# Kernel optimization log

Measured on AMD Instinct MI355X. Metric: run time of the kernel, lower is better.

## Reference

```python
import jax, jax.numpy as jnp
import numpy as np

# Module constants (match init_kwargs)
IMG_W = 384
IMG_H = 384
DECAY = 0.97
VEH_W = 2.1
VEH_L = 4.9
PPM = 5
LIGHT_OFF_X = 12.0
LIGHT_OFF_Y = 3.25
ALPHA = 1.1


def create_coordinate_mask(nx, ny, ppm):
    # Metric coordinates of every BEV pixel, ego frame origin at image center.
    xs = (jnp.arange(nx, dtype=jnp.float32) - nx / 2.0) / ppm
    ys = (jnp.arange(ny, dtype=jnp.float32) - ny / 2.0) / ppm
    X, Y = jnp.meshgrid(xs, ys)  # (ny, nx)
    return jnp.stack([X, Y], axis=-1)  # (H, W, 2)


def rotate_batched(location, yaw):
    # Express future poses (t=1..T-1) in the frame of the pose at t=0.
    loc0 = location[:, :1]              # (B,1,2)
    yaw0 = yaw[:, :1]                   # (B,1,1)
    rel = location[:, 1:] - loc0        # (B,T-1,2)
    c, s = jnp.cos(yaw0), jnp.sin(yaw0)
    x = c * rel[..., 0:1] + s * rel[..., 1:2]    # (B,T-1,1)
    y = -s * rel[..., 0:1] + c * rel[..., 1:2]   # (B,T-1,1)
    return x, y, yaw[:, 1:] - yaw0


def align_with_ego(x, y, yaw, cm):
    # Translate grid to ego position then rotate into ego heading frame.
    # x,y,yaw: (B,T-1,1); cm: (H,W,2). Returns two (B,T-1,H,W) coord fields.
    relx = cm[..., 0][None, None] - x[..., None]   # (B,T-1,H,W)
    rely = cm[..., 1][None, None] - y[..., None]
    c = jnp.cos(yaw)[..., None]
    s = jnp.sin(yaw)[..., None]
    ax = c * relx + s * rely
    ay = -s * relx + c * rely
    return ax, ay


def calculate_mask(ax, ay, dx, dy, vw, vl, alpha):
    dtype = ax.dtype
    # Speed-dependent corridor ahead of the vehicle.
    mask_car = ((jnp.abs(ax) <= dx) & (ay >= 0.0) & (ay <= dy)).astype(dtype)
    # Inflated vehicle footprint (for lane / offroad costs).
    mask_side = ((jnp.abs(ax) <= alpha * vw / 2.0)
                 & (jnp.abs(ay) <= alpha * vl / 2.0)).astype(dtype)
    return mask_car, mask_side


def setup_inputs() -> dict:
    key = jax.random.key(0)
    k1, k2, k3, k4 = jax.random.split(key, 4)
    B, T = 8, 11
    location = jax.random.normal(k1, (B, T, 2), dtype=jnp.float32) * 5.0
    yaw = jax.random.normal(k2, (B, T, 1), dtype=jnp.float32) * 0.3
    speed = jax.random.uniform(k3, (B, T, 1), dtype=jnp.float32) * 15.0
    bev = jax.random.uniform(k4, (B, T, 8, IMG_H, IMG_W), dtype=jnp.float32)
    return {"location": location, "yaw": yaw, "speed": speed, "bev": bev}


def reference(location, yaw, speed, bev):
    cm = create_coordinate_mask(IMG_W, IMG_H, PPM)   # (H,W,2)
    x, y, yaw_ = rotate_batched(location, yaw)        # (B,T-1,1) each
    speed_ = speed[:, 1:, 0:1]                        # (B,T-1,1)

    ax, ay = align_with_ego(x, y, yaw_, cm)
    axl, ayl = align_with_ego(x + LIGHT_OFF_X, y + LIGHT_OFF_Y, yaw_, cm)

    dx = VEH_W / 2.0 + 4.0
    dx_light = VEH_W + 1.0
    dy = (1.5 * (jnp.maximum(10.0, speed_) + VEH_L) + 1.0)[..., None]  # (B,T-1,1,1)
    dy_light = (speed_ * 0.5 + VEH_L * 3.0)[..., None]                  # (B,T-1,1,1)

    mask_car, mask_side = calculate_mask(ax, ay, dx, dy, VEH_W, VEH_L, ALPHA)
    mask_light, _ = calculate_mask(axl, ayl, dx_light, dy_light, VEH_W, VEH_L, ALPHA)

    # Binarize BEV at 0.5 (matches the in-place > / <= thresholding).
    bev_b = (bev[:, 1:] > 0.5).astype(bev.dtype)  # (B,T-1,8,H,W)

    Tm1 = bev_b.shape[1]
    decay = jnp.power(jnp.float32(DECAY),
                      jnp.arange(Tm1, dtype=jnp.float32)).reshape(1, Tm1, 1, 1)

    def cost(chan, mask):
        return jnp.sum(bev_b[:, :, chan] * mask * decay)

    lane_cost = cost(1, mask_side)
    vehicle_cost = cost(2, mask_car)
    green_light_cost = cost(3, mask_light)
    yellow_light_cost = cost(4, mask_light)
    red_light_cost = cost(5, mask_light)
    pedestrian_cost = cost(6, mask_car)
    offroad_cost = cost(7, mask_side)

    return (lane_cost, vehicle_cost, green_light_cost, yellow_light_cost,
            red_light_cost, pedestrian_cost, offroad_cost,
            mask_car, mask_side, mask_light)
```

## Files before the change

kernel.cpp:

```cpp
#include <hip/hip_runtime.h>
#include <math.h>

constexpr int IMG     = 384;
constexpr int NPIX    = IMG * IMG;
constexpr int TM1     = 10;
constexpr int NIMG    = 80;
constexpr int THREADS = 256;
constexpr int GPT     = 4;
constexpr int GPB     = THREADS * GPT;
constexpr int NGRP    = NPIX / 4;
constexpr int NBX     = NGRP / GPB;
constexpr int NSUM    = 12;
constexpr long long NMASK = (long long)NIMG * NPIX;

typedef float v4f __attribute__((ext_vector_type(4)));


__global__ __launch_bounds__(THREADS) void cost_main(
    const float* __restrict__ loc,
    const float* __restrict__ yaw,
    const float* __restrict__ speed,
    const float* __restrict__ bev,
    float* __restrict__ out)
{
    const int img = blockIdx.y;
    const int b   = img / TM1;
    const int t   = img - b * TM1;
    const int tid = threadIdx.x;

    const float yaw0 = yaw[b * 11];
    const float c0 = cosf(yaw0), s0 = sinf(yaw0);
    const float rx = loc[(b * 11 + t + 1) * 2 + 0] - loc[b * 22 + 0];
    const float ry = loc[(b * 11 + t + 1) * 2 + 1] - loc[b * 22 + 1];
    const float x0 =  c0 * rx + s0 * ry;
    const float y0 = -s0 * rx + c0 * ry;
    const float yw = yaw[b * 11 + t + 1] - yaw0;
    const float c = cosf(yw), s = sinf(yw);
    const float sp  = speed[b * 11 + t + 1];
    const float dy  = 1.5f * (fmaxf(10.0f, sp) + 4.9f) + 1.0f;
    const float dyl = sp * 0.5f + 14.7f;
    const float ox  = 12.0f * c + 3.25f * s;
    const float oy  = 12.0f * s - 3.25f * c;

    if (blockIdx.x < NBX) {
        float* ocar   = out + 7 + (size_t)img * NPIX;
        float* oside  = ocar + NMASK;
        float* olight = ocar + 2 * NMASK;

        const int g0 = blockIdx.x * GPB + tid;
        #pragma unroll
        for (int it = 0; it < GPT; ++it) {
            const int g = g0 + it * THREADS;
            if (g != NGRP - 1) {
                const int pb = 4 * g + 1;
                float mc[4], ms[4], ml[4];
                #pragma unroll
                for (int k = 0; k < 4; ++k) {
                    const int p = pb + k;
                    const int i = p / IMG;
                    const int j = p - i * IMG;
                    const float X = (float)j * 0.2f - 38.4f;
                    const float Y = (float)i * 0.2f - 38.4f;
                    const float relx = X - x0, rely = Y - y0;
                    const float ax = c * relx + s * rely;
                    const float ay = c * rely - s * relx;
                    const float axl = ax - ox, ayl = ay + oy;
                    mc[k] = (fabsf(ax)  <= 5.05f  && ay >= 0.f && ay <= dy)   ? 1.f : 0.f;
                    ms[k] = (fabsf(ax)  <= 1.155f && fabsf(ay) <= 2.695f)     ? 1.f : 0.f;
                    ml[k] = (fabsf(axl) <= 3.1f   && ayl >= 0.f && ayl <= dyl)? 1.f : 0.f;
                }
                v4f vc = {mc[0], mc[1], mc[2], mc[3]};
                v4f vs = {ms[0], ms[1], ms[2], ms[3]};
                v4f vl = {ml[0], ml[1], ml[2], ml[3]};
                *(v4f*)(ocar + pb)   = vc;
                *(v4f*)(oside + pb)  = vs;
                *(v4f*)(olight + pb) = vl;
            } else {
                const int pp[4] = {0, NPIX - 3, NPIX - 2, NPIX - 1};
                for (int k = 0; k < 4; ++k) {
                    const int p = pp[k];
                    const int i = p / IMG;
                    const int j = p - i * IMG;
                    const float X = (float)j * 0.2f - 38.4f;
                    const float Y = (float)i * 0.2f - 38.4f;
                    const float relx = X - x0, rely = Y - y0;
                    const float ax = c * relx + s * rely;
                    const float ay = c * rely - s * relx;
                    const float axl = ax - ox, ayl = ay + oy;
                    ocar[p]   = (fabsf(ax)  <= 5.05f  && ay >= 0.f && ay <= dy)    ? 1.f : 0.f;
                    oside[p]  = (fabsf(ax)  <= 1.155f && fabsf(ay) <= 2.695f)      ? 1.f : 0.f;
                    olight[p] = (fabsf(axl) <= 3.1f   && ayl >= 0.f && ayl <= dyl) ? 1.f : 0.f;
                }
            }
        }
        return;
    }

    const int q   = blockIdx.x - NBX;
    const int reg = q >> 2;
    const int z   = q & 3;

    const float* bp = bev + (size_t)((b * 11 + t + 1) * 8) * NPIX;

    float u0, u1, v0, v1;
    if (reg == 0)      { u0 = -5.05f;      u1 = 5.05f;      v0 = 0.f;      v1 = dy; }
    else if (reg == 1) { u0 = -1.155f;     u1 = 1.155f;     v0 = -2.695f;  v1 = 2.695f; }
    else               { u0 = ox - 3.1f;   u1 = ox + 3.1f;  v0 = -oy;      v1 = dyl - oy; }

    float Xmn = 1e30f, Xmx = -1e30f, Ymn = 1e30f, Ymx = -1e30f;
    #pragma unroll
    for (int cu = 0; cu < 2; ++cu)
        #pragma unroll
        for (int cv = 0; cv < 2; ++cv) {
            const float u = cu ? u1 : u0, v = cv ? v1 : v0;
            const float X = x0 + c * u - s * v;
            const float Y = y0 + s * u + c * v;
            Xmn = fminf(Xmn, X); Xmx = fmaxf(Xmx, X);
            Ymn = fminf(Ymn, Y); Ymx = fmaxf(Ymx, Y);
        }
    const int j0 = max(0, (int)floorf((Xmn + 38.4f) * 5.f) - 1);
    const int j1 = min(IMG - 1, (int)ceilf((Xmx + 38.4f) * 5.f) + 1);
    const int i0 = max(0, (int)floorf((Ymn + 38.4f) * 5.f) - 1);
    const int i1 = min(IMG - 1, (int)ceilf((Ymx + 38.4f) * 5.f) + 1);

    float a0 = 0.f, a1 = 0.f, a2 = 0.f;

    if (j1 >= j0 && i1 >= i0) {
        const int w = j1 - j0 + 1;
        const int n = w * (i1 - i0 + 1);
        for (int idx = tid + z * THREADS; idx < n; idx += 4 * THREADS) {
            const int ii = idx / w;
            const int jj = j0 + (idx - ii * w);
            const int i  = i0 + ii;
            const float X = (float)jj * 0.2f - 38.4f;
            const float Y = (float)i  * 0.2f - 38.4f;
            const float relx = X - x0, rely = Y - y0;
            const float ax = c * relx + s * rely;
            const float ay = c * rely - s * relx;
            const int p = i * IMG + jj;
            if (reg == 0) {
                if (fabsf(ax) <= 5.05f && ay >= 0.f && ay <= dy) {
                    a0 += (bp[2 * NPIX + p] > 0.5f) ? 1.f : 0.f;
                    a1 += (bp[6 * NPIX + p] > 0.5f) ? 1.f : 0.f;
                }
            } else if (reg == 1) {
                if (fabsf(ax) <= 1.155f && fabsf(ay) <= 2.695f) {
                    a0 += (bp[1 * NPIX + p] > 0.5f) ? 1.f : 0.f;
                    a1 += (bp[7 * NPIX + p] > 0.5f) ? 1.f : 0.f;
                }
            } else {
                const float axl = ax - ox, ayl = ay + oy;
                if (fabsf(axl) <= 3.1f && ayl >= 0.f && ayl <= dyl) {
                    a0 += (bp[3 * NPIX + p] > 0.5f) ? 1.f : 0.f;
                    a1 += (bp[4 * NPIX + p] > 0.5f) ? 1.f : 0.f;
                    a2 += (bp[5 * NPIX + p] > 0.5f) ? 1.f : 0.f;
                }
            }
        }
    }

    float acc[3] = {a0, a1, a2};
    #pragma unroll
    for (int k = 0; k < 3; ++k) {
        #pragma unroll
        for (int off = 32; off > 0; off >>= 1)
            acc[k] += __shfl_down(acc[k], off, 64);
    }
    __shared__ float red[4][3];
    const int wid = tid >> 6, lane = tid & 63;
    if (lane == 0) {
        #pragma unroll
        for (int k = 0; k < 3; ++k) red[wid][k] = acc[k];
    }
    __syncthreads();
    if (tid < 3) {
        const float v = red[0][tid] + red[1][tid] + red[2][tid] + red[3][tid];
        if (v != 0.0f) {
            float decay = 1.0f;
            for (int qd = 0; qd < t; ++qd) decay *= 0.97f;
            int slot;
            if (reg == 0)      slot = (tid == 0) ? 1 : 5;
            else if (reg == 1) slot = (tid == 0) ? 0 : 6;
            else               slot = 2 + tid;
            if (reg == 2 || tid < 2)
                atomicAdd(&out[slot], v * decay);
        }
    }
}

extern "C" void kernel_launch(void* const* d_in, const int* in_sizes, int n_in,
                              void* d_out, int out_size, void* d_ws, size_t ws_size,
                              hipStream_t stream) {
    const float* loc   = (const float*)d_in[0];
    const float* yaw   = (const float*)d_in[1];
    const float* speed = (const float*)d_in[2];
    const float* bev   = (const float*)d_in[3];
    float* out = (float*)d_out;

    (void)hipMemsetAsync(d_out, 0, 7 * sizeof(float), stream);

    dim3 grid(NBX + NSUM, NIMG);
    cost_main<<<grid, THREADS, 0, stream>>>(loc, yaw, speed, bev, out);
}
```

Measured before the change: 38.33 us.

## Replace dense mask writes with memset plus sparse writes inside bounding boxes

Drops the dense pass that evaluated and wrote every pixel of the three mask outputs. Instead the whole output buffer is zeroed with hipMemsetAsync, and the region-sum blocks write 1.0 only for the pixels inside each mask while they accumulate costs. The grid becomes images x regions x 4 slices. Mask writes are now scattered, uncoalesced stores, and the memset still has to write the full ~35 MB output, so the write bandwidth cost remains, just moved to the memset path.

```diff
diff --git a/kernel.cpp b/kernel.cpp
--- a/kernel.cpp
+++ b/kernel.cpp
@@ -6,24 +6,19 @@
 constexpr int TM1     = 10;
 constexpr int NIMG    = 80;
 constexpr int THREADS = 256;
-constexpr int GPT     = 4;
-constexpr int GPB     = THREADS * GPT;
-constexpr int NGRP    = NPIX / 4;
-constexpr int NBX     = NGRP / GPB;
-constexpr int NSUM    = 12;
 constexpr long long NMASK = (long long)NIMG * NPIX;
 
-typedef float v4f __attribute__((ext_vector_type(4)));
 
-
-__global__ __launch_bounds__(THREADS) void cost_main(
+__global__ __launch_bounds__(THREADS) void cost_regions(
     const float* __restrict__ loc,
     const float* __restrict__ yaw,
     const float* __restrict__ speed,
     const float* __restrict__ bev,
     float* __restrict__ out)
 {
-    const int img = blockIdx.y;
+    const int img = blockIdx.x;
+    const int reg = blockIdx.y;
+    const int z   = blockIdx.z;
     const int b   = img / TM1;
     const int t   = img - b * TM1;
     const int tid = threadIdx.x;
@@ -42,65 +37,8 @@
     const float ox  = 12.0f * c + 3.25f * s;
     const float oy  = 12.0f * s - 3.25f * c;
 
-    if (blockIdx.x < NBX) {
-        float* ocar   = out + 7 + (size_t)img * NPIX;
-        float* oside  = ocar + NMASK;
-        float* olight = ocar + 2 * NMASK;
-
-        const int g0 = blockIdx.x * GPB + tid;
-        #pragma unroll
-        for (int it = 0; it < GPT; ++it) {
-            const int g = g0 + it * THREADS;
-            if (g != NGRP - 1) {
-                const int pb = 4 * g + 1;
-                float mc[4], ms[4], ml[4];
-                #pragma unroll
-                for (int k = 0; k < 4; ++k) {
-                    const int p = pb + k;
-                    const int i = p / IMG;
-                    const int j = p - i * IMG;
-                    const float X = (float)j * 0.2f - 38.4f;
-                    const float Y = (float)i * 0.2f - 38.4f;
-                    const float relx = X - x0, rely = Y - y0;
-                    const float ax = c * relx + s * rely;
-                    const float ay = c * rely - s * relx;
-                    const float axl = ax - ox, ayl = ay + oy;
-                    mc[k] = (fabsf(ax)  <= 5.05f  && ay >= 0.f && ay <= dy)   ? 1.f : 0.f;
-                    ms[k] = (fabsf(ax)  <= 1.155f && fabsf(ay) <= 2.695f)     ? 1.f : 0.f;
-                    ml[k] = (fabsf(axl) <= 3.1f   && ayl >= 0.f && ayl <= dyl)? 1.f : 0.f;
-                }
-                v4f vc = {mc[0], mc[1], mc[2], mc[3]};
-                v4f vs = {ms[0], ms[1], ms[2], ms[3]};
-                v4f vl = {ml[0], ml[1], ml[2], ml[3]};
-                *(v4f*)(ocar + pb)   = vc;
-                *(v4f*)(oside + pb)  = vs;
-                *(v4f*)(olight + pb) = vl;
-            } else {
-                const int pp[4] = {0, NPIX - 3, NPIX - 2, NPIX - 1};
-                for (int k = 0; k < 4; ++k) {
-                    const int p = pp[k];
-                    const int i = p / IMG;
-                    const int j = p - i * IMG;
-                    const float X = (float)j * 0.2f - 38.4f;
-                    const float Y = (float)i * 0.2f - 38.4f;
-                    const float relx = X - x0, rely = Y - y0;
-                    const float ax = c * relx + s * rely;
-                    const float ay = c * rely - s * relx;
-                    const float axl = ax - ox, ayl = ay + oy;
-                    ocar[p]   = (fabsf(ax)  <= 5.05f  && ay >= 0.f && ay <= dy)    ? 1.f : 0.f;
-                    oside[p]  = (fabsf(ax)  <= 1.155f && fabsf(ay) <= 2.695f)      ? 1.f : 0.f;
-                    olight[p] = (fabsf(axl) <= 3.1f   && ayl >= 0.f && ayl <= dyl) ? 1.f : 0.f;
-                }
-            }
-        }
-        return;
-    }
-
-    const int q   = blockIdx.x - NBX;
-    const int reg = q >> 2;
-    const int z   = q & 3;
-
     const float* bp = bev + (size_t)((b * 11 + t + 1) * 8) * NPIX;
+    float* op = out + 7 + (size_t)img * NPIX + (size_t)reg * NMASK;
 
     float u0, u1, v0, v1;
     if (reg == 0)      { u0 = -5.05f;      u1 = 5.05f;      v0 = 0.f;      v1 = dy; }
@@ -140,17 +78,20 @@
             const int p = i * IMG + jj;
             if (reg == 0) {
                 if (fabsf(ax) <= 5.05f && ay >= 0.f && ay <= dy) {
+                    op[p] = 1.0f;
                     a0 += (bp[2 * NPIX + p] > 0.5f) ? 1.f : 0.f;
                     a1 += (bp[6 * NPIX + p] > 0.5f) ? 1.f : 0.f;
                 }
             } else if (reg == 1) {
                 if (fabsf(ax) <= 1.155f && fabsf(ay) <= 2.695f) {
+                    op[p] = 1.0f;
                     a0 += (bp[1 * NPIX + p] > 0.5f) ? 1.f : 0.f;
                     a1 += (bp[7 * NPIX + p] > 0.5f) ? 1.f : 0.f;
                 }
             } else {
                 const float axl = ax - ox, ayl = ay + oy;
                 if (fabsf(axl) <= 3.1f && ayl >= 0.f && ayl <= dyl) {
+                    op[p] = 1.0f;
                     a0 += (bp[3 * NPIX + p] > 0.5f) ? 1.f : 0.f;
                     a1 += (bp[4 * NPIX + p] > 0.5f) ? 1.f : 0.f;
                     a2 += (bp[5 * NPIX + p] > 0.5f) ? 1.f : 0.f;
@@ -197,8 +138,8 @@
     const float* bev   = (const float*)d_in[3];
     float* out = (float*)d_out;
 
-    (void)hipMemsetAsync(d_out, 0, 7 * sizeof(float), stream);
+    (void)hipMemsetAsync(d_out, 0, (size_t)out_size * sizeof(float), stream);
 
-    dim3 grid(NBX + NSUM, NIMG);
-    cost_main<<<grid, THREADS, 0, stream>>>(loc, yaw, speed, bev, out);
+    dim3 grid(NIMG, 3, 4);
+    cost_regions<<<grid, THREADS, 0, stream>>>(loc, yaw, speed, bev, out);
 }
```

Measured after the change: 42.77 us. 11.6% more time.

## Flatten grid, schedule reduction blocks first and coarsen mask-writer blocks

Applied to the files above, without the earlier changes.

Replaces the 2D grid with a 1D grid in which all 960 bbox-reduction blocks come first and are dispatched early, followed by mask-writing blocks that each process four chunks instead of one. Putting the latency-bound gather/reduction blocks at the front lets them overlap with the bandwidth-bound mask stores instead of trailing behind them. Coarsening cuts the mask block count by four, at the cost of recomputing the per-image pose parameters (including sin/cos) in every unit and leaving fewer blocks to hide latency.

```diff
diff --git a/kernel.cpp b/kernel.cpp
--- a/kernel.cpp
+++ b/kernel.cpp
@@ -9,8 +9,11 @@
 constexpr int GPT     = 4;
 constexpr int GPB     = THREADS * GPT;
 constexpr int NGRP    = NPIX / 4;
-constexpr int NBX     = NGRP / GPB;
-constexpr int NSUM    = 12;
+constexpr int CHUNKS  = NGRP / GPB;
+constexpr int NUNITS  = NIMG * CHUNKS;
+constexpr int UPB     = 4;
+constexpr int NSTRB   = NUNITS / UPB;
+constexpr int NSUMB   = NIMG * 12;
 constexpr long long NMASK = (long long)NIMG * NPIX;
 
 typedef float v4f __attribute__((ext_vector_type(4)));
@@ -23,31 +26,147 @@
     const float* __restrict__ bev,
     float* __restrict__ out)
 {
-    const int img = blockIdx.y;
-    const int b   = img / TM1;
-    const int t   = img - b * TM1;
     const int tid = threadIdx.x;
 
-    const float yaw0 = yaw[b * 11];
-    const float c0 = cosf(yaw0), s0 = sinf(yaw0);
-    const float rx = loc[(b * 11 + t + 1) * 2 + 0] - loc[b * 22 + 0];
-    const float ry = loc[(b * 11 + t + 1) * 2 + 1] - loc[b * 22 + 1];
-    const float x0 =  c0 * rx + s0 * ry;
-    const float y0 = -s0 * rx + c0 * ry;
-    const float yw = yaw[b * 11 + t + 1] - yaw0;
-    const float c = cosf(yw), s = sinf(yw);
-    const float sp  = speed[b * 11 + t + 1];
-    const float dy  = 1.5f * (fmaxf(10.0f, sp) + 4.9f) + 1.0f;
-    const float dyl = sp * 0.5f + 14.7f;
-    const float ox  = 12.0f * c + 3.25f * s;
-    const float oy  = 12.0f * s - 3.25f * c;
-
-    if (blockIdx.x < NBX) {
+    if (blockIdx.x < NSUMB) {
+        const int img = blockIdx.x / 12;
+        const int q   = blockIdx.x - img * 12;
+        const int reg = q >> 2;
+        const int z   = q & 3;
+        const int b   = img / TM1;
+        const int t   = img - b * TM1;
+
+        const float yaw0 = yaw[b * 11];
+        const float c0 = cosf(yaw0), s0 = sinf(yaw0);
+        const float rx = loc[(b * 11 + t + 1) * 2 + 0] - loc[b * 22 + 0];
+        const float ry = loc[(b * 11 + t + 1) * 2 + 1] - loc[b * 22 + 1];
+        const float x0 =  c0 * rx + s0 * ry;
+        const float y0 = -s0 * rx + c0 * ry;
+        const float yw = yaw[b * 11 + t + 1] - yaw0;
+        const float c = cosf(yw), s = sinf(yw);
+        const float sp  = speed[b * 11 + t + 1];
+        const float dy  = 1.5f * (fmaxf(10.0f, sp) + 4.9f) + 1.0f;
+        const float dyl = sp * 0.5f + 14.7f;
+        const float ox  = 12.0f * c + 3.25f * s;
+        const float oy  = 12.0f * s - 3.25f * c;
+
+        const float* bp = bev + (size_t)((b * 11 + t + 1) * 8) * NPIX;
+
+        float u0, u1, v0, v1;
+        if (reg == 0)      { u0 = -5.05f;      u1 = 5.05f;      v0 = 0.f;      v1 = dy; }
+        else if (reg == 1) { u0 = -1.155f;     u1 = 1.155f;     v0 = -2.695f;  v1 = 2.695f; }
+        else               { u0 = ox - 3.1f;   u1 = ox + 3.1f;  v0 = -oy;      v1 = dyl - oy; }
+
+        float Xmn = 1e30f, Xmx = -1e30f, Ymn = 1e30f, Ymx = -1e30f;
+        #pragma unroll
+        for (int cu = 0; cu < 2; ++cu)
+            #pragma unroll
+            for (int cv = 0; cv < 2; ++cv) {
+                const float u = cu ? u1 : u0, v = cv ? v1 : v0;
+                const float X = x0 + c * u - s * v;
+                const float Y = y0 + s * u + c * v;
+                Xmn = fminf(Xmn, X); Xmx = fmaxf(Xmx, X);
+                Ymn = fminf(Ymn, Y); Ymx = fmaxf(Ymx, Y);
+            }
+        const int j0 = max(0, (int)floorf((Xmn + 38.4f) * 5.f) - 1);
+        const int j1 = min(IMG - 1, (int)ceilf((Xmx + 38.4f) * 5.f) + 1);
+        const int i0 = max(0, (int)floorf((Ymn + 38.4f) * 5.f) - 1);
+        const int i1 = min(IMG - 1, (int)ceilf((Ymx + 38.4f) * 5.f) + 1);
+
+        float a0 = 0.f, a1 = 0.f, a2 = 0.f;
+
+        if (j1 >= j0 && i1 >= i0) {
+            const int w = j1 - j0 + 1;
+            const int n = w * (i1 - i0 + 1);
+            for (int idx = tid + z * THREADS; idx < n; idx += 4 * THREADS) {
+                const int ii = idx / w;
+                const int jj = j0 + (idx - ii * w);
+                const int i  = i0 + ii;
+                const float X = (float)jj * 0.2f - 38.4f;
+                const float Y = (float)i  * 0.2f - 38.4f;
+                const float relx = X - x0, rely = Y - y0;
+                const float ax = c * relx + s * rely;
+                const float ay = c * rely - s * relx;
+                const int p = i * IMG + jj;
+                if (reg == 0) {
+                    if (fabsf(ax) <= 5.05f && ay >= 0.f && ay <= dy) {
+                        a0 += (bp[2 * NPIX + p] > 0.5f) ? 1.f : 0.f;
+                        a1 += (bp[6 * NPIX + p] > 0.5f) ? 1.f : 0.f;
+                    }
+                } else if (reg == 1) {
+                    if (fabsf(ax) <= 1.155f && fabsf(ay) <= 2.695f) {
+                        a0 += (bp[1 * NPIX + p] > 0.5f) ? 1.f : 0.f;
+                        a1 += (bp[7 * NPIX + p] > 0.5f) ? 1.f : 0.f;
+                    }
+                } else {
+                    const float axl = ax - ox, ayl = ay + oy;
+                    if (fabsf(axl) <= 3.1f && ayl >= 0.f && ayl <= dyl) {
+                        a0 += (bp[3 * NPIX + p] > 0.5f) ? 1.f : 0.f;
+                        a1 += (bp[4 * NPIX + p] > 0.5f) ? 1.f : 0.f;
+                        a2 += (bp[5 * NPIX + p] > 0.5f) ? 1.f : 0.f;
+                    }
+                }
+            }
+        }
+
+        float acc[3] = {a0, a1, a2};
+        #pragma unroll
+        for (int k = 0; k < 3; ++k) {
+            #pragma unroll
+            for (int off = 32; off > 0; off >>= 1)
+                acc[k] += __shfl_down(acc[k], off, 64);
+        }
+        __shared__ float red[4][3];
+        const int wid = tid >> 6, lane = tid & 63;
+        if (lane == 0) {
+            #pragma unroll
+            for (int k = 0; k < 3; ++k) red[wid][k] = acc[k];
+        }
+        __syncthreads();
+        if (tid < 3) {
+            const float v = red[0][tid] + red[1][tid] + red[2][tid] + red[3][tid];
+            if (v != 0.0f) {
+                float decay = 1.0f;
+                for (int qd = 0; qd < t; ++qd) decay *= 0.97f;
+                int slot;
+                if (reg == 0)      slot = (tid == 0) ? 1 : 5;
+                else if (reg == 1) slot = (tid == 0) ? 0 : 6;
+                else               slot = 2 + tid;
+                if (reg == 2 || tid < 2)
+                    atomicAdd(&out[slot], v * decay);
+            }
+        }
+        return;
+    }
+
+    const int sid = blockIdx.x - NSUMB;
+    #pragma unroll
+    for (int uu = 0; uu < UPB; ++uu) {
+        const int u     = sid * UPB + uu;
+        const int img   = u / CHUNKS;
+        const int chunk = u - img * CHUNKS;
+        const int b     = img / TM1;
+        const int t     = img - b * TM1;
+
+        const float yaw0 = yaw[b * 11];
+        const float c0 = cosf(yaw0), s0 = sinf(yaw0);
+        const float rx = loc[(b * 11 + t + 1) * 2 + 0] - loc[b * 22 + 0];
+        const float ry = loc[(b * 11 + t + 1) * 2 + 1] - loc[b * 22 + 1];
+        const float x0 =  c0 * rx + s0 * ry;
+        const float y0 = -s0 * rx + c0 * ry;
+        const float yw = yaw[b * 11 + t + 1] - yaw0;
+        const float c = cosf(yw), s = sinf(yw);
+        const float sp  = speed[b * 11 + t + 1];
+        const float dy  = 1.5f * (fmaxf(10.0f, sp) + 4.9f) + 1.0f;
+        const float dyl = sp * 0.5f + 14.7f;
+        const float ox  = 12.0f * c + 3.25f * s;
+        const float oy  = 12.0f * s - 3.25f * c;
+
         float* ocar   = out + 7 + (size_t)img * NPIX;
         float* oside  = ocar + NMASK;
         float* olight = ocar + 2 * NMASK;
 
-        const int g0 = blockIdx.x * GPB + tid;
+        const int g0 = chunk * GPB + tid;
         #pragma unroll
         for (int it = 0; it < GPT; ++it) {
             const int g = g0 + it * THREADS;
@@ -93,98 +212,6 @@
                 }
             }
         }
-        return;
-    }
-
-    const int q   = blockIdx.x - NBX;
-    const int reg = q >> 2;
-    const int z   = q & 3;
-
-    const float* bp = bev + (size_t)((b * 11 + t + 1) * 8) * NPIX;
-
-    float u0, u1, v0, v1;
-    if (reg == 0)      { u0 = -5.05f;      u1 = 5.05f;      v0 = 0.f;      v1 = dy; }
-    else if (reg == 1) { u0 = -1.155f;     u1 = 1.155f;     v0 = -2.695f;  v1 = 2.695f; }
-    else               { u0 = ox - 3.1f;   u1 = ox + 3.1f;  v0 = -oy;      v1 = dyl - oy; }
-
-    float Xmn = 1e30f, Xmx = -1e30f, Ymn = 1e30f, Ymx = -1e30f;
-    #pragma unroll
-    for (int cu = 0; cu < 2; ++cu)
-        #pragma unroll
-        for (int cv = 0; cv < 2; ++cv) {
-            const float u = cu ? u1 : u0, v = cv ? v1 : v0;
-            const float X = x0 + c * u - s * v;
-            const float Y = y0 + s * u + c * v;
-            Xmn = fminf(Xmn, X); Xmx = fmaxf(Xmx, X);
-            Ymn = fminf(Ymn, Y); Ymx = fmaxf(Ymx, Y);
-        }
-    const int j0 = max(0, (int)floorf((Xmn + 38.4f) * 5.f) - 1);
-    const int j1 = min(IMG - 1, (int)ceilf((Xmx + 38.4f) * 5.f) + 1);
-    const int i0 = max(0, (int)floorf((Ymn + 38.4f) * 5.f) - 1);
-    const int i1 = min(IMG - 1, (int)ceilf((Ymx + 38.4f) * 5.f) + 1);
-
-    float a0 = 0.f, a1 = 0.f, a2 = 0.f;
-
-    if (j1 >= j0 && i1 >= i0) {
-        const int w = j1 - j0 + 1;
-        const int n = w * (i1 - i0 + 1);
-        for (int idx = tid + z * THREADS; idx < n; idx += 4 * THREADS) {
-            const int ii = idx / w;
-            const int jj = j0 + (idx - ii * w);
-            const int i  = i0 + ii;
-            const float X = (float)jj * 0.2f - 38.4f;
-            const float Y = (float)i  * 0.2f - 38.4f;
-            const float relx = X - x0, rely = Y - y0;
-            const float ax = c * relx + s * rely;
-            const float ay = c * rely - s * relx;
-            const int p = i * IMG + jj;
-            if (reg == 0) {
-                if (fabsf(ax) <= 5.05f && ay >= 0.f && ay <= dy) {
-                    a0 += (bp[2 * NPIX + p] > 0.5f) ? 1.f : 0.f;
-                    a1 += (bp[6 * NPIX + p] > 0.5f) ? 1.f : 0.f;
-                }
-            } else if (reg == 1) {
-                if (fabsf(ax) <= 1.155f && fabsf(ay) <= 2.695f) {
-                    a0 += (bp[1 * NPIX + p] > 0.5f) ? 1.f : 0.f;
-                    a1 += (bp[7 * NPIX + p] > 0.5f) ? 1.f : 0.f;
-                }
-            } else {
-                const float axl = ax - ox, ayl = ay + oy;
-                if (fabsf(axl) <= 3.1f && ayl >= 0.f && ayl <= dyl) {
-                    a0 += (bp[3 * NPIX + p] > 0.5f) ? 1.f : 0.f;
-                    a1 += (bp[4 * NPIX + p] > 0.5f) ? 1.f : 0.f;
-                    a2 += (bp[5 * NPIX + p] > 0.5f) ? 1.f : 0.f;
-                }
-            }
-        }
-    }
-
-    float acc[3] = {a0, a1, a2};
-    #pragma unroll
-    for (int k = 0; k < 3; ++k) {
-        #pragma unroll
-        for (int off = 32; off > 0; off >>= 1)
-            acc[k] += __shfl_down(acc[k], off, 64);
-    }
-    __shared__ float red[4][3];
-    const int wid = tid >> 6, lane = tid & 63;
-    if (lane == 0) {
-        #pragma unroll
-        for (int k = 0; k < 3; ++k) red[wid][k] = acc[k];
-    }
-    __syncthreads();
-    if (tid < 3) {
-        const float v = red[0][tid] + red[1][tid] + red[2][tid] + red[3][tid];
-        if (v != 0.0f) {
-            float decay = 1.0f;
-            for (int qd = 0; qd < t; ++qd) decay *= 0.97f;
-            int slot;
-            if (reg == 0)      slot = (tid == 0) ? 1 : 5;
-            else if (reg == 1) slot = (tid == 0) ? 0 : 6;
-            else               slot = 2 + tid;
-            if (reg == 2 || tid < 2)
-                atomicAdd(&out[slot], v * decay);
-        }
     }
 }
 
@@ -199,6 +226,6 @@
 
     (void)hipMemsetAsync(d_out, 0, 7 * sizeof(float), stream);
 
-    dim3 grid(NBX + NSUM, NIMG);
+    dim3 grid(NSUMB + NSTRB, 1);
     cost_main<<<grid, THREADS, 0, stream>>>(loc, yaw, speed, bev, out);
 }
```

Measured after the change: 37.12 us. 3.2% less time.
